# Kernel tuning notes

Measured on AMD Instinct MI355X. Metric: run time of the kernel, lower is better.

Reference implementation:

```python
import jax, jax.numpy as jnp
import numpy as np

BLANK = 0
NEG = -1e30  # safe -inf surrogate for log-domain DP


def _ctc_loss_mean(pred, label, label_length):
    # pred: [B, T, C] raw logits; label: [B, Lmax] int; label_length: [B] int
    B, T, C = pred.shape
    Lmax = label.shape[1]
    S = 2 * Lmax + 1

    logp = jax.nn.log_softmax(pred.astype(jnp.float32), axis=-1)  # [B, T, C]

    # extended label sequence: blank, l1, blank, l2, ..., blank  -> [B, S]
    ext = jnp.full((B, S), BLANK, dtype=label.dtype)
    ext = ext.at[:, 1::2].set(label)
    prev2 = jnp.pad(ext[:, :-2], ((0, 0), (2, 0)), constant_values=BLANK)
    skip = (ext != BLANK) & (ext != prev2) & (jnp.arange(S) >= 2)  # [B, S]

    # gather log-probs of extended labels per time step: [T, B, S]
    lp = jnp.transpose(logp, (1, 0, 2))  # [T, B, C]
    lp_ext = jnp.take_along_axis(
        lp, jnp.broadcast_to(ext[None].astype(jnp.int32), (T, B, S)), axis=2)

    # alpha recursion (forward DP in log space)
    alpha0 = jnp.full((B, S), NEG, dtype=jnp.float32)
    alpha0 = alpha0.at[:, 0].set(lp_ext[0, :, 0])
    alpha0 = alpha0.at[:, 1].set(lp_ext[0, :, 1])

    def step(alpha, lp_t):
        s1 = jnp.pad(alpha[:, :-1], ((0, 0), (1, 0)), constant_values=NEG)
        s2 = jnp.pad(alpha[:, :-2], ((0, 0), (2, 0)), constant_values=NEG)
        a = jnp.logaddexp(alpha, s1)
        a = jnp.where(skip, jnp.logaddexp(a, s2), a)
        return a + lp_t, None

    alpha, _ = jax.lax.scan(step, alpha0, lp_ext[1:])  # [B, S]

    # total log-likelihood: last blank (s=2L) or last label (s=2L-1)
    L = label_length.astype(jnp.int32)
    a_last = jnp.take_along_axis(alpha, (2 * L)[:, None], axis=1)[:, 0]
    a_prev = jnp.take_along_axis(alpha, (2 * L - 1)[:, None], axis=1)[:, 0]
    loss = -jnp.logaddexp(a_last, a_prev)  # [B]

    # torch CTCLoss(reduction='mean'): mean over batch of loss / target_length
    return jnp.mean(loss / L.astype(jnp.float32))


def setup_inputs() -> dict:
    key = jax.random.key(0)
    k1, k2, k3 = jax.random.split(key, 3)
    B, T, C, Lmax = 128, 128, 6625, 25
    pred = jax.random.normal(k1, (B, T, C), dtype=jnp.float32)
    label = jax.random.randint(k2, (B, Lmax), 1, C, dtype=jnp.int32)
    label_length = jax.random.randint(k3, (B,), 1, Lmax + 1, dtype=jnp.int32)
    return {"pred": pred, "label": label, "label_length": label_length}


def reference(pred, label, label_length):
    return _ctc_loss_mean(pred, label, label_length)
```

## Files before the change

kernel.cpp:

```cpp
#include <hip/hip_runtime.h>
#include <hip/hip_bf16.h>

#define NEGINF (-1e30f)

constexpr int Bsz  = 128;
constexpr int Tlen = 128;
constexpr int Ccls = 6625;
constexpr int Lmax = 25;
constexpr int Sext = 2 * Lmax + 1;

__global__ __launch_bounds__(256) void lse_gather_kernel(
        const float* __restrict__ pred,
        const int*   __restrict__ label,
        float*       __restrict__ lp_ext) {
    const int bt  = blockIdx.x;
    const int b   = bt / Tlen;
    const int tid = threadIdx.x;
    const float* row = pred + (size_t)bt * Ccls;

    uintptr_t addr = (uintptr_t)row;
    const int head = (int)(((16u - (unsigned)(addr & 15u)) & 15u) >> 2);
    const int n4   = (Ccls - head) >> 2;
    const int tail_start = head + (n4 << 2);

    const float4* row4 = (const float4*)(row + head);

    float4 v[7];
    #pragma unroll
    for (int it = 0; it < 6; ++it) v[it] = row4[tid + it * 256];
    {
        int i = tid + 6 * 256;
        v[6] = (i < n4) ? row4[i] : make_float4(NEGINF, NEGINF, NEGINF, NEGINF);
    }
    float hv = (tid < head) ? row[tid] : NEGINF;
    int ti = tail_start + tid;
    float tv = (ti < Ccls) ? row[ti] : NEGINF;

    float gval = 0.0f;
    if (tid < Sext) {
        int cls = (tid & 1) ? label[b * Lmax + (tid >> 1)] : 0;
        gval = row[cls];
    }

    float s0 = 0.f, s1 = 0.f, s2 = 0.f, s3 = 0.f;
    #pragma unroll
    for (int it = 0; it < 7; ++it) {
        s0 += __expf(v[it].x);
        s1 += __expf(v[it].y);
        s2 += __expf(v[it].z);
        s3 += __expf(v[it].w);
    }
    s0 += __expf(hv);
    s1 += __expf(tv);
    float s = (s0 + s1) + (s2 + s3);

    #pragma unroll
    for (int off = 32; off > 0; off >>= 1) s += __shfl_xor(s, off);
    __shared__ float red[4];
    const int wave = tid >> 6, lane = tid & 63;
    if (lane == 0) red[wave] = s;
    __syncthreads();
    const float Sv = (red[0] + red[1]) + (red[2] + red[3]);
    const float logZ = __logf(Sv);

    if (tid < Sext)
        lp_ext[(size_t)bt * Sext + tid] = gval - logZ;
}

__global__ __launch_bounds__(128) void ctc_dp_kernel(
        const float* __restrict__ lp_ext,
        const int*   __restrict__ label,
        const int*   __restrict__ lablen,
        float*       __restrict__ loss) {
    const int b   = blockIdx.x;
    const int tid = threadIdx.x;

    __shared__ float lp[Tlen * Sext];
    const float4* src4 = (const float4*)(lp_ext + (size_t)b * Tlen * Sext);
    float4* dst4 = (float4*)lp;
    constexpr int N4 = (Tlen * Sext) / 4;
    #pragma unroll
    for (int it = 0; it < (N4 + 127) / 128; ++it) {
        int i = tid + it * 128;
        if (i < N4) dst4[i] = src4[i];
    }
    __syncthreads();

    if (tid < 64) {
        const int lane = tid;

        bool skip = false;
        if ((lane & 1) && lane >= 3 && lane < Sext) {
            int k = lane >> 1;
            skip = (label[b * Lmax + k] != label[b * Lmax + k - 1]);
        }
        const bool live = (lane < Sext);

        float alpha = NEGINF;
        if (live && lane <= 1) alpha = lp[lane];

        #pragma unroll 4
        for (int t = 1; t < Tlen; ++t) {
            float lpt = live ? lp[t * Sext + lane] : NEGINF;
            float s1 = __shfl_up(alpha, 1);
            float s2 = __shfl_up(alpha, 2);
            if (lane < 1) s1 = NEGINF;
            if (!skip)    s2 = NEGINF;
            float M = fmaxf(fmaxf(alpha, s1), s2);
            float sum = __expf(alpha - M) + __expf(s1 - M) + __expf(s2 - M);
            alpha = M + __logf(sum) + lpt;
        }

        __shared__ float al[64];
        al[lane] = alpha;
        __builtin_amdgcn_s_barrier();
        if (lane == 0) {
            int L = lablen[b];
            float a = al[2 * L], p = al[2 * L - 1];
            float M = fmaxf(a, p);
            float ll = M + __logf(__expf(a - M) + __expf(p - M));
            loss[b] = -ll / (float)L;
        }
    }
}

__global__ __launch_bounds__(128) void reduce_mean_kernel(
        const float* __restrict__ loss, float* __restrict__ out) {
    const int tid = threadIdx.x;
    float v = loss[tid];
    #pragma unroll
    for (int off = 32; off > 0; off >>= 1) v += __shfl_xor(v, off);
    __shared__ float ws[2];
    if ((tid & 63) == 0) ws[tid >> 6] = v;
    __syncthreads();
    if (tid == 0) out[0] = (ws[0] + ws[1]) * (1.0f / (float)Bsz);
}

extern "C" void kernel_launch(void* const* d_in, const int* in_sizes, int n_in,
                              void* d_out, int out_size, void* d_ws, size_t ws_size,
                              hipStream_t stream) {
    const float* pred   = (const float*)d_in[0];
    const int*   label  = (const int*)d_in[1];
    const int*   lablen = (const int*)d_in[2];
    float* out = (float*)d_out;

    float* lp_ext = (float*)d_ws;
    float* loss   = (float*)((char*)d_ws +
                     (size_t)Bsz * Tlen * Sext * sizeof(float));

    lse_gather_kernel<<<Bsz * Tlen, 256, 0, stream>>>(pred, label, lp_ext);
    ctc_dp_kernel<<<Bsz, 128, 0, stream>>>(lp_ext, label, lablen, loss);
    reduce_mean_kernel<<<1, 128, 0, stream>>>(loss, out);
}
```

Before: 99.28 us.

## Persistent software-pipelined LSE rows and fuse mean reduction via atomics

The log-softmax/gather kernel now launches 2048 blocks that each process 8 rows, double-buffering the register loads so the next row's loads are in flight while the current row is being reduced. The final mean reduction kernel is removed: the DP kernel reads the end alphas with shuffles and atomically accumulates each scaled loss into the output, which the first kernel zeroes. This trades a kernel launch and more memory-level parallelism for higher register pressure, and makes the floating-point summation order nondeterministic.

```diff
diff --git a/kernel.cpp b/kernel.cpp
--- a/kernel.cpp
+++ b/kernel.cpp
@@ -8,70 +8,92 @@
 constexpr int Ccls = 6625;
 constexpr int Lmax = 25;
 constexpr int Sext = 2 * Lmax + 1;
+constexpr int NBLK = 2048;
+constexpr int GENS = (Bsz * Tlen) / NBLK;
 
-__global__ __launch_bounds__(256) void lse_gather_kernel(
+__global__ __launch_bounds__(256, 4) void lse_gather_kernel(
         const float* __restrict__ pred,
         const int*   __restrict__ label,
-        float*       __restrict__ lp_ext) {
-    const int bt  = blockIdx.x;
-    const int b   = bt / Tlen;
+        float*       __restrict__ lp_ext,
+        float*       __restrict__ out) {
+    const int bid = blockIdx.x;
     const int tid = threadIdx.x;
-    const float* row = pred + (size_t)bt * Ccls;
+    const int wave = tid >> 6, lane = tid & 63;
 
-    uintptr_t addr = (uintptr_t)row;
-    const int head = (int)(((16u - (unsigned)(addr & 15u)) & 15u) >> 2);
-    const int n4   = (Ccls - head) >> 2;
-    const int tail_start = head + (n4 << 2);
-
-    const float4* row4 = (const float4*)(row + head);
-
-    float4 v[7];
-    #pragma unroll
-    for (int it = 0; it < 6; ++it) v[it] = row4[tid + it * 256];
-    {
-        int i = tid + 6 * 256;
-        v[6] = (i < n4) ? row4[i] : make_float4(NEGINF, NEGINF, NEGINF, NEGINF);
-    }
-    float hv = (tid < head) ? row[tid] : NEGINF;
-    int ti = tail_start + tid;
-    float tv = (ti < Ccls) ? row[ti] : NEGINF;
-
-    float gval = 0.0f;
+    int cls[GENS];
     if (tid < Sext) {
-        int cls = (tid & 1) ? label[b * Lmax + (tid >> 1)] : 0;
-        gval = row[cls];
+        #pragma unroll
+        for (int g = 0; g < GENS; ++g) {
+            int bg = (bid + g * NBLK) >> 7;
+            cls[g] = (tid & 1) ? label[bg * Lmax + (tid >> 1)] : 0;
+        }
     }
 
-    float s0 = 0.f, s1 = 0.f, s2 = 0.f, s3 = 0.f;
-    #pragma unroll
-    for (int it = 0; it < 7; ++it) {
-        s0 += __expf(v[it].x);
-        s1 += __expf(v[it].y);
-        s2 += __expf(v[it].z);
-        s3 += __expf(v[it].w);
-    }
-    s0 += __expf(hv);
-    s1 += __expf(tv);
-    float s = (s0 + s1) + (s2 + s3);
+    __shared__ float red[GENS][4];
 
-    #pragma unroll
-    for (int off = 32; off > 0; off >>= 1) s += __shfl_xor(s, off);
-    __shared__ float red[4];
-    const int wave = tid >> 6, lane = tid & 63;
-    if (lane == 0) red[wave] = s;
-    __syncthreads();
-    const float Sv = (red[0] + red[1]) + (red[2] + red[3]);
-    const float logZ = __logf(Sv);
+    float4 va[7], vb[7];
+    float hva, tva, gva, hvb, tvb, gvb;
 
-    if (tid < Sext)
-        lp_ext[(size_t)bt * Sext + tid] = gval - logZ;
+    #define LOADROW(g, V, HV, TV, GV) do {                                   \
+        const float* row_ = pred + (size_t)(bid + (g) * NBLK) * Ccls;        \
+        uintptr_t a_ = (uintptr_t)row_;                                      \
+        const int head_ = (int)(((16u - (unsigned)(a_ & 15u)) & 15u) >> 2);  \
+        const int n4_ = (Ccls - head_) >> 2;                                 \
+        const float4* r4_ = (const float4*)(row_ + head_);                   \
+        _Pragma("unroll")                                                    \
+        for (int it_ = 0; it_ < 6; ++it_) V[it_] = r4_[tid + it_ * 256];     \
+        { int i_ = tid + 6 * 256;                                            \
+          V[6] = (i_ < n4_) ? r4_[i_]                                        \
+                            : make_float4(NEGINF, NEGINF, NEGINF, NEGINF); } \
+        HV = (tid < head_) ? row_[tid] : NEGINF;                             \
+        { int ti_ = head_ + (n4_ << 2) + tid;                                \
+          TV = (ti_ < Ccls) ? row_[ti_] : NEGINF; }                          \
+        GV = 0.0f;                                                           \
+        if (tid < Sext) GV = row_[cls[(g)]];                                 \
+    } while (0)
+
+    #define CONSUME(g, V, HV, TV, GV) do {                                   \
+        float s0 = 0.f, s1 = 0.f, s2 = 0.f, s3 = 0.f;                        \
+        _Pragma("unroll")                                                    \
+        for (int it_ = 0; it_ < 7; ++it_) {                                  \
+            s0 += __expf(V[it_].x); s1 += __expf(V[it_].y);                  \
+            s2 += __expf(V[it_].z); s3 += __expf(V[it_].w);                  \
+        }                                                                    \
+        s0 += __expf(HV); s1 += __expf(TV);                                  \
+        float s_ = (s0 + s1) + (s2 + s3);                                    \
+        _Pragma("unroll")                                                    \
+        for (int off_ = 32; off_ > 0; off_ >>= 1)                            \
+            s_ += __shfl_xor(s_, off_);                                      \
+        if (lane == 0) red[(g)][wave] = s_;                                  \
+        __syncthreads();                                                     \
+        const float Sv_ = (red[(g)][0] + red[(g)][1])                        \
+                        + (red[(g)][2] + red[(g)][3]);                       \
+        if (tid < Sext)                                                      \
+            lp_ext[(size_t)(bid + (g) * NBLK) * Sext + tid]                  \
+                = GV - __logf(Sv_);                                          \
+    } while (0)
+
+    LOADROW(0, va, hva, tva, gva);
+    LOADROW(1, vb, hvb, tvb, gvb);  CONSUME(0, va, hva, tva, gva);
+    LOADROW(2, va, hva, tva, gva);  CONSUME(1, vb, hvb, tvb, gvb);
+    LOADROW(3, vb, hvb, tvb, gvb);  CONSUME(2, va, hva, tva, gva);
+    LOADROW(4, va, hva, tva, gva);  CONSUME(3, vb, hvb, tvb, gvb);
+    LOADROW(5, vb, hvb, tvb, gvb);  CONSUME(4, va, hva, tva, gva);
+    LOADROW(6, va, hva, tva, gva);  CONSUME(5, vb, hvb, tvb, gvb);
+    LOADROW(7, vb, hvb, tvb, gvb);  CONSUME(6, va, hva, tva, gva);
+    CONSUME(7, vb, hvb, tvb, gvb);
+
+    #undef LOADROW
+    #undef CONSUME
+
+    if (bid == 0 && tid == 0) out[0] = 0.0f;
 }
 
 __global__ __launch_bounds__(128) void ctc_dp_kernel(
         const float* __restrict__ lp_ext,
         const int*   __restrict__ label,
         const int*   __restrict__ lablen,
-        float*       __restrict__ loss) {
+        float*       __restrict__ out) {
     const int b   = blockIdx.x;
     const int tid = threadIdx.x;
 
@@ -111,29 +133,15 @@
             alpha = M + __logf(sum) + lpt;
         }
 
-        __shared__ float al[64];
-        al[lane] = alpha;
-        __builtin_amdgcn_s_barrier();
+        int L = lablen[b];
+        float a = __shfl(alpha, 2 * L);
+        float p = __shfl(alpha, 2 * L - 1);
         if (lane == 0) {
-            int L = lablen[b];
-            float a = al[2 * L], p = al[2 * L - 1];
             float M = fmaxf(a, p);
             float ll = M + __logf(__expf(a - M) + __expf(p - M));
-            loss[b] = -ll / (float)L;
+            atomicAdd(out, -ll / (float)L * (1.0f / (float)Bsz));
         }
     }
-}
-
-__global__ __launch_bounds__(128) void reduce_mean_kernel(
-        const float* __restrict__ loss, float* __restrict__ out) {
-    const int tid = threadIdx.x;
-    float v = loss[tid];
-    #pragma unroll
-    for (int off = 32; off > 0; off >>= 1) v += __shfl_xor(v, off);
-    __shared__ float ws[2];
-    if ((tid & 63) == 0) ws[tid >> 6] = v;
-    __syncthreads();
-    if (tid == 0) out[0] = (ws[0] + ws[1]) * (1.0f / (float)Bsz);
 }
 
 extern "C" void kernel_launch(void* const* d_in, const int* in_sizes, int n_in,
@@ -145,10 +153,7 @@
     float* out = (float*)d_out;
 
     float* lp_ext = (float*)d_ws;
-    float* loss   = (float*)((char*)d_ws +
-                     (size_t)Bsz * Tlen * Sext * sizeof(float));
 
-    lse_gather_kernel<<<Bsz * Tlen, 256, 0, stream>>>(pred, label, lp_ext);
-    ctc_dp_kernel<<<Bsz, 128, 0, stream>>>(lp_ext, label, lablen, loss);
-    reduce_mean_kernel<<<1, 128, 0, stream>>>(loss, out);
+    lse_gather_kernel<<<NBLK, 256, 0, stream>>>(pred, label, lp_ext, out);
+    ctc_dp_kernel<<<Bsz, 128, 0, stream>>>(lp_ext, label, lablen, out);
 }
```

Result: slower. 106.0 us (+6.8%).

## Drop reduce kernel via atomic mean, simplify row loads with masked aligned window

Applied to the files above, without the earlier changes.

The final mean reduction kernel is removed. Each CTC DP block now atomically adds its scaled loss into the output, which the LSE kernel zeroes first. The LSE kernel loads an aligned float4 window covering each row and masks out-of-row elements, replacing the separate head/tail scalar loads, and adds an occupancy hint to launch bounds. The per-block shared-memory barrier for the final alpha lookup is replaced with shuffles. This saves a kernel launch and some scalar loads, but makes the summation order nondeterministic.

```diff
diff --git a/kernel.cpp b/kernel.cpp
--- a/kernel.cpp
+++ b/kernel.cpp
@@ -9,49 +9,46 @@
 constexpr int Lmax = 25;
 constexpr int Sext = 2 * Lmax + 1;
 
-__global__ __launch_bounds__(256) void lse_gather_kernel(
+__global__ __launch_bounds__(256, 8) void lse_gather_kernel(
         const float* __restrict__ pred,
         const int*   __restrict__ label,
-        float*       __restrict__ lp_ext) {
+        float*       __restrict__ lp_ext,
+        float*       __restrict__ out) {
     const int bt  = blockIdx.x;
-    const int b   = bt / Tlen;
     const int tid = threadIdx.x;
-    const float* row = pred + (size_t)bt * Ccls;
 
-    uintptr_t addr = (uintptr_t)row;
-    const int head = (int)(((16u - (unsigned)(addr & 15u)) & 15u) >> 2);
-    const int n4   = (Ccls - head) >> 2;
-    const int tail_start = head + (n4 << 2);
+    const size_t row_start = (size_t)bt * Ccls;
+    const size_t w0   = row_start & ~(size_t)3;
+    const int    lead = (int)(row_start - w0);
+    const float4* win = (const float4*)(pred + w0);
 
-    const float4* row4 = (const float4*)(row + head);
+    float gval = 0.0f;
+    if (tid < Sext) {
+        int b = bt >> 7;
+        int cls = (tid & 1) ? label[b * Lmax + (tid >> 1)] : 0;
+        gval = pred[row_start + cls];
+    }
 
     float4 v[7];
     #pragma unroll
-    for (int it = 0; it < 6; ++it) v[it] = row4[tid + it * 256];
-    {
-        int i = tid + 6 * 256;
-        v[6] = (i < n4) ? row4[i] : make_float4(NEGINF, NEGINF, NEGINF, NEGINF);
-    }
-    float hv = (tid < head) ? row[tid] : NEGINF;
-    int ti = tail_start + tid;
-    float tv = (ti < Ccls) ? row[ti] : NEGINF;
+    for (int it = 0; it < 6; ++it) v[it] = win[tid + it * 256];
+    if (tid < 121) v[6] = win[tid + 6 * 256];
+    else           v[6] = make_float4(NEGINF, NEGINF, NEGINF, NEGINF);
 
-    float gval = 0.0f;
-    if (tid < Sext) {
-        int cls = (tid & 1) ? label[b * Lmax + (tid >> 1)] : 0;
-        gval = row[cls];
-    }
-
+    const int ebase0 = tid * 4 - lead;
     float s0 = 0.f, s1 = 0.f, s2 = 0.f, s3 = 0.f;
     #pragma unroll
     for (int it = 0; it < 7; ++it) {
-        s0 += __expf(v[it].x);
-        s1 += __expf(v[it].y);
-        s2 += __expf(v[it].z);
-        s3 += __expf(v[it].w);
+        int e = ebase0 + it * 1024;
+        float x0 = ((unsigned)(e + 0) < (unsigned)Ccls) ? v[it].x : NEGINF;
+        float x1 = ((unsigned)(e + 1) < (unsigned)Ccls) ? v[it].y : NEGINF;
+        float x2 = ((unsigned)(e + 2) < (unsigned)Ccls) ? v[it].z : NEGINF;
+        float x3 = ((unsigned)(e + 3) < (unsigned)Ccls) ? v[it].w : NEGINF;
+        s0 += __expf(x0);
+        s1 += __expf(x1);
+        s2 += __expf(x2);
+        s3 += __expf(x3);
     }
-    s0 += __expf(hv);
-    s1 += __expf(tv);
     float s = (s0 + s1) + (s2 + s3);
 
     #pragma unroll
@@ -61,17 +58,18 @@
     if (lane == 0) red[wave] = s;
     __syncthreads();
     const float Sv = (red[0] + red[1]) + (red[2] + red[3]);
-    const float logZ = __logf(Sv);
 
     if (tid < Sext)
-        lp_ext[(size_t)bt * Sext + tid] = gval - logZ;
+        lp_ext[(size_t)bt * Sext + tid] = gval - __logf(Sv);
+
+    if (bt == 0 && tid == 0) out[0] = 0.0f;
 }
 
 __global__ __launch_bounds__(128) void ctc_dp_kernel(
         const float* __restrict__ lp_ext,
         const int*   __restrict__ label,
         const int*   __restrict__ lablen,
-        float*       __restrict__ loss) {
+        float*       __restrict__ out) {
     const int b   = blockIdx.x;
     const int tid = threadIdx.x;
 
@@ -111,29 +109,15 @@
             alpha = M + __logf(sum) + lpt;
         }
 
-        __shared__ float al[64];
-        al[lane] = alpha;
-        __builtin_amdgcn_s_barrier();
+        int L = lablen[b];
+        float a = __shfl(alpha, 2 * L);
+        float p = __shfl(alpha, 2 * L - 1);
         if (lane == 0) {
-            int L = lablen[b];
-            float a = al[2 * L], p = al[2 * L - 1];
             float M = fmaxf(a, p);
             float ll = M + __logf(__expf(a - M) + __expf(p - M));
-            loss[b] = -ll / (float)L;
+            atomicAdd(out, -ll / (float)L * (1.0f / (float)Bsz));
         }
     }
-}
-
-__global__ __launch_bounds__(128) void reduce_mean_kernel(
-        const float* __restrict__ loss, float* __restrict__ out) {
-    const int tid = threadIdx.x;
-    float v = loss[tid];
-    #pragma unroll
-    for (int off = 32; off > 0; off >>= 1) v += __shfl_xor(v, off);
-    __shared__ float ws[2];
-    if ((tid & 63) == 0) ws[tid >> 6] = v;
-    __syncthreads();
-    if (tid == 0) out[0] = (ws[0] + ws[1]) * (1.0f / (float)Bsz);
 }
 
 extern "C" void kernel_launch(void* const* d_in, const int* in_sizes, int n_in,
@@ -145,10 +129,7 @@
     float* out = (float*)d_out;
 
     float* lp_ext = (float*)d_ws;
-    float* loss   = (float*)((char*)d_ws +
-                     (size_t)Bsz * Tlen * Sext * sizeof(float));
 
-    lse_gather_kernel<<<Bsz * Tlen, 256, 0, stream>>>(pred, label, lp_ext);
-    ctc_dp_kernel<<<Bsz, 128, 0, stream>>>(lp_ext, label, lablen, loss);
-    reduce_mean_kernel<<<1, 128, 0, stream>>>(loss, out);
+    lse_gather_kernel<<<Bsz * Tlen, 256, 0, stream>>>(pred, label, lp_ext, out);
+    ctc_dp_kernel<<<Bsz, 128, 0, stream>>>(lp_ext, label, lablen, out);
 }
```

Result: faster. 96.44 us (-2.9%).
